# Optimization experiments

Measured on AMD Instinct MI355X. Metric: run time of the kernel, lower is better.

## Reference

```python
import jax, jax.numpy as jnp
import numpy as np

N_VOX = 200000   # active voxels
K = 27           # 3x3x3 kernel offsets
P = 100000       # rulebook pairs per kernel offset
C_IN = 64
C_OUT = 64
BN_EPS = 1e-5


def setup_inputs() -> dict:
    key = jax.random.key(0)
    k1, k2, k3, k4, k5 = jax.random.split(key, 5)
    features = jax.random.normal(k1, (N_VOX, C_IN), dtype=jnp.float32)
    weight = jax.random.normal(k2, (K, C_IN, C_OUT), dtype=jnp.float32) * 0.05
    bias = jax.random.normal(k3, (C_OUT,), dtype=jnp.float32) * 0.05
    gamma = jnp.ones((C_OUT,), dtype=jnp.float32)
    beta = jnp.zeros((C_OUT,), dtype=jnp.float32)
    in_idx = jax.random.randint(k4, (K, P), 0, N_VOX, dtype=jnp.int32)
    out_idx = jax.random.randint(k5, (K, P), 0, N_VOX, dtype=jnp.int32)
    return {"features": features, "weight": weight, "bias": bias,
            "gamma": gamma, "beta": beta, "in_idx": in_idx, "out_idx": out_idx}


def reference(features, weight, bias, gamma, beta, in_idx, out_idx):
    # --- sparse submanifold conv: gather -> per-offset GEMM -> scatter-add ---
    gathered = features[in_idx]                         # [K, P, C_in]
    partial = jnp.einsum('kpc,kcd->kpd', gathered, weight)  # [K, P, C_out]
    out = jnp.zeros((N_VOX, C_OUT), dtype=features.dtype)
    out = out.at[out_idx.reshape(-1)].add(partial.reshape(-1, C_OUT))
    out = out + bias                                    # conv bias
    # --- BatchNorm1d (training mode: batch stats, biased variance) ---
    mean = jnp.mean(out, axis=0)
    var = jnp.mean(jnp.square(out - mean), axis=0)
    normed = (out - mean) * jax.lax.rsqrt(var + BN_EPS) * gamma + beta
    # --- ReLU ---
    return jnp.maximum(normed, 0.0)
```

## Files before the change

### kernel.cpp

```cpp
#include <hip/hip_runtime.h>
#include <hip/hip_bf16.h>

#define N_VOX 200000
#define KOFF 27
#define PPK 100000
#define C 64
#define BN_EPS 1e-5f

typedef __bf16 bf16x8 __attribute__((ext_vector_type(8)));
typedef __bf16 bf16x4 __attribute__((ext_vector_type(4)));
typedef float f32x4 __attribute__((ext_vector_type(4)));

__global__ __launch_bounds__(256)
void convert_features(const float* __restrict__ f, __bf16* __restrict__ fb)
{
    const size_t total4 = (size_t)N_VOX * C / 4;
    const size_t i = (size_t)blockIdx.x * blockDim.x + threadIdx.x;
    if (i >= total4) return;
    const float4 v = ((const float4*)f)[i];
    bf16x4 o;
    o.x = (__bf16)v.x; o.y = (__bf16)v.y; o.z = (__bf16)v.z; o.w = (__bf16)v.w;
    ((bf16x4*)fb)[i] = o;
}

__global__ __launch_bounds__(256)
void convert_weight(const float* __restrict__ w, __bf16* __restrict__ wt)
{
    const int k = blockIdx.x;
    const float* W = w + (size_t)k * C * C;
    __bf16* Wt = wt + (size_t)k * C * C;
    for (int idx = threadIdx.x; idx < C * C; idx += 256) {
        const int ci = idx >> 6, co = idx & 63;
        Wt[co * C + ci] = (__bf16)W[idx];
    }
}

__global__ __launch_bounds__(256)
void hist_kernel(const int* __restrict__ out_idx, unsigned* __restrict__ counts,
                 int k0, int npair)
{
    const int i = blockIdx.x * 256 + threadIdx.x;
    if (i < npair) {
        const int o = out_idx[(size_t)k0 * PPK + i];
        atomicAdd(&counts[o], 1u);
    }
}

__global__ __launch_bounds__(256)
void scan1(const unsigned* __restrict__ counts, unsigned* __restrict__ offsets,
           unsigned* __restrict__ bsums)
{
    __shared__ unsigned sdata[256];
    const int t = threadIdx.x;
    const int base = blockIdx.x * 1024 + t * 4;
    unsigned v[4]; unsigned s = 0;
#pragma unroll
    for (int u = 0; u < 4; ++u) {
        v[u] = (base + u < N_VOX) ? counts[base + u] : 0u;
        s += v[u];
    }
    sdata[t] = s;
    __syncthreads();
    for (int off = 1; off < 256; off <<= 1) {
        const unsigned add = (t >= off) ? sdata[t - off] : 0u;
        __syncthreads();
        sdata[t] += add;
        __syncthreads();
    }
    const unsigned incl = sdata[t];
    unsigned run = incl - s;
    if (t == 255) bsums[blockIdx.x] = incl;
#pragma unroll
    for (int u = 0; u < 4; ++u) {
        if (base + u < N_VOX) offsets[base + u] = run;
        run += v[u];
    }
}

__global__ __launch_bounds__(256)
void scan2(unsigned* __restrict__ bsums, int nb)
{
    __shared__ unsigned sdata[256];
    const int t = threadIdx.x;
    const unsigned s = (t < nb) ? bsums[t] : 0u;
    sdata[t] = s;
    __syncthreads();
    for (int off = 1; off < 256; off <<= 1) {
        const unsigned add = (t >= off) ? sdata[t - off] : 0u;
        __syncthreads();
        sdata[t] += add;
        __syncthreads();
    }
    if (t < nb) bsums[t] = sdata[t] - s;
}

__global__ __launch_bounds__(256)
void scan3(unsigned* __restrict__ offsets, const unsigned* __restrict__ bsums,
           unsigned* __restrict__ cursor)
{
    const int i = blockIdx.x * 256 + threadIdx.x;
    if (i < N_VOX) {
        const unsigned v = offsets[i] + bsums[i >> 10];
        offsets[i] = v;
        cursor[i] = v;
    }
}

__global__ __launch_bounds__(256)
void rank_fill(const int* __restrict__ out_idx, unsigned* __restrict__ cursor,
               unsigned* __restrict__ rank, int k0, int npair)
{
    const int i = blockIdx.x * 256 + threadIdx.x;
    if (i < npair) {
        const int o = out_idx[(size_t)k0 * PPK + i];
        rank[i] = atomicAdd(&cursor[o], 1u);
    }
}

__global__ __launch_bounds__(256)
void conv_scatter(const __bf16* __restrict__ featb, const __bf16* __restrict__ wtb,
                  const int* __restrict__ in_idx, const unsigned* __restrict__ rank,
                  __bf16* __restrict__ partial, int k0)
{
    constexpr int TP = 256;
    constexpr int STRIDE = 72;
    __shared__ __bf16 sA[TP * STRIDE];
    __shared__ unsigned s_rank[TP];

    const int kloc = blockIdx.y;
    const int k = k0 + kloc;
    const int tile_base = blockIdx.x * TP;
    const int t = threadIdx.x;
    const int lane = t & 63;
    const int wave = t >> 6;
    const int m16 = lane & 15;
    const int quad = lane >> 4;

    const __bf16* Wt = wtb + (size_t)k * C * C;
    bf16x8 bfrag[4][2];
#pragma unroll
    for (int nt = 0; nt < 4; ++nt)
#pragma unroll
        for (int kc = 0; kc < 2; ++kc)
            bfrag[nt][kc] = *(const bf16x8*)(Wt + (nt * 16 + m16) * C + kc * 32 + quad * 8);

    {
        const int pair = tile_base + t;
        s_rank[t] = (pair < PPK) ? rank[(size_t)kloc * PPK + pair] : 0u;
    }

    const int c8 = t & 7;
    const int r0 = t >> 3;
#pragma unroll
    for (int it = 0; it < 8; ++it) {
        const int r = r0 + it * 32;
        const int pair = tile_base + r;
        const int row = (pair < PPK) ? in_idx[(size_t)k * PPK + pair] : 0;
        const float4 v = *(const float4*)(featb + (size_t)row * C + c8 * 8);
        *(float4*)(sA + r * STRIDE + c8 * 8) = v;
    }
    __syncthreads();

    f32x4 acc[4][4] = {};
    const int mbase = wave * 64;
#pragma unroll
    for (int kc = 0; kc < 2; ++kc) {
        bf16x8 afrag[4];
#pragma unroll
        for (int mt = 0; mt < 4; ++mt)
            afrag[mt] = *(const bf16x8*)(sA + (mbase + mt * 16 + m16) * STRIDE + kc * 32 + quad * 8);
#pragma unroll
        for (int nt = 0; nt < 4; ++nt)
#pragma unroll
            for (int mt = 0; mt < 4; ++mt)
                acc[mt][nt] = __builtin_amdgcn_mfma_f32_16x16x32_bf16(
                    afrag[mt], bfrag[nt][kc], acc[mt][nt], 0, 0, 0);
    }

#pragma unroll
    for (int mt = 0; mt < 4; ++mt) {
#pragma unroll
        for (int reg = 0; reg < 4; ++reg) {
            const int r = mbase + mt * 16 + quad * 4 + reg;
            const int pair = tile_base + r;
            if (pair < PPK) {
                const unsigned slot = s_rank[r];
                bf16x4 pv;
                pv.x = (__bf16)acc[mt][0][reg];
                pv.y = (__bf16)acc[mt][1][reg];
                pv.z = (__bf16)acc[mt][2][reg];
                pv.w = (__bf16)acc[mt][3][reg];
                *(bf16x4*)(partial + (size_t)slot * C + (m16 << 2)) = pv;
            }
        }
    }
}

__global__ __launch_bounds__(256)
void reduce_kernel(const __bf16* __restrict__ partial,
                   const unsigned* __restrict__ offsets,
                   const unsigned* __restrict__ counts,
                   float* __restrict__ out, const int first)
{
    const int t = threadIdx.x;
    const int j = t & 15;
    const int i = t >> 4;
    const int o = blockIdx.x * 16 + i;
    const unsigned beg = offsets[o];
    const unsigned cnt = counts[o];
    float a0, a1, a2, a3;
    if (first) {
        a0 = a1 = a2 = a3 = 0.f;
    } else {
        a0 = out[(size_t)o * C + j];
        a1 = out[(size_t)o * C + 16 + j];
        a2 = out[(size_t)o * C + 32 + j];
        a3 = out[(size_t)o * C + 48 + j];
    }
    const __bf16* base = partial + (size_t)beg * C + (j << 2);
    for (unsigned e = 0; e < cnt; ++e) {
        const bf16x4 v = *(const bf16x4*)(base + (size_t)e * C);
        a0 += (float)v.x; a1 += (float)v.y; a2 += (float)v.z; a3 += (float)v.w;
    }
    out[(size_t)o * C + j]      = a0;
    out[(size_t)o * C + 16 + j] = a1;
    out[(size_t)o * C + 32 + j] = a2;
    out[(size_t)o * C + 48 + j] = a3;
}

__global__ __launch_bounds__(256)
void conv_mfma(const __bf16* __restrict__ featb, const __bf16* __restrict__ wtb,
               const int* __restrict__ in_idx, const int* __restrict__ out_idx,
               float* __restrict__ out)
{
    constexpr int TP = 256;
    constexpr int STRIDE = 72;
    __shared__ __bf16 sA[TP * STRIDE];
    __shared__ int s_out[TP];

    const int k = blockIdx.y;
    const int tile_base = blockIdx.x * TP;
    const int t = threadIdx.x;
    const int lane = t & 63;
    const int wave = t >> 6;
    const int m16 = lane & 15;
    const int quad = lane >> 4;

    const __bf16* Wt = wtb + (size_t)k * C * C;
    bf16x8 bfrag[4][2];
#pragma unroll
    for (int nt = 0; nt < 4; ++nt)
#pragma unroll
        for (int kc = 0; kc < 2; ++kc)
            bfrag[nt][kc] = *(const bf16x8*)(Wt + (nt * 16 + m16) * C + kc * 32 + quad * 8);

    {
        const int pair = tile_base + t;
        s_out[t] = (pair < PPK) ? out_idx[(size_t)k * PPK + pair] : 0;
    }

    const int c8 = t & 7;
    const int r0 = t >> 3;
#pragma unroll
    for (int it = 0; it < 8; ++it) {
        const int r = r0 + it * 32;
        const int pair = tile_base + r;
        const int row = (pair < PPK) ? in_idx[(size_t)k * PPK + pair] : 0;
        const float4 v = *(const float4*)(featb + (size_t)row * C + c8 * 8);
        *(float4*)(sA + r * STRIDE + c8 * 8) = v;
    }
    __syncthreads();

    f32x4 acc[4][4] = {};
    const int mbase = wave * 64;
#pragma unroll
    for (int kc = 0; kc < 2; ++kc) {
        bf16x8 afrag[4];
#pragma unroll
        for (int mt = 0; mt < 4; ++mt)
            afrag[mt] = *(const bf16x8*)(sA + (mbase + mt * 16 + m16) * STRIDE + kc * 32 + quad * 8);
#pragma unroll
        for (int nt = 0; nt < 4; ++nt)
#pragma unroll
            for (int mt = 0; mt < 4; ++mt)
                acc[mt][nt] = __builtin_amdgcn_mfma_f32_16x16x32_bf16(
                    afrag[mt], bfrag[nt][kc], acc[mt][nt], 0, 0, 0);
    }

#pragma unroll
    for (int mt = 0; mt < 4; ++mt) {
#pragma unroll
        for (int reg = 0; reg < 4; ++reg) {
            const int r = mbase + mt * 16 + quad * 4 + reg;
            const int pair = tile_base + r;
            if (pair < PPK) {
                const int o = s_out[r];
                float* orow = out + (size_t)o * C + m16;
#pragma unroll
                for (int nt = 0; nt < 4; ++nt)
                    unsafeAtomicAdd(orow + nt * 16, acc[mt][nt][reg]);
            }
        }
    }
}

__global__ __launch_bounds__(256)
void stats_kernel(const float* __restrict__ out,
                  float* __restrict__ stats,
                  int rows_per_block)
{
    __shared__ float ssum[256];
    __shared__ float ssq[256];
    const int c   = threadIdx.x & 63;
    const int sub = threadIdx.x >> 6;
    const int row0 = blockIdx.x * rows_per_block;
    const int row1 = min(row0 + rows_per_block, N_VOX);
    float s = 0.f, q = 0.f;
    for (int r = row0 + sub; r < row1; r += 4) {
        const float v = out[(size_t)r * C + c];
        s += v;
        q += v * v;
    }
    ssum[threadIdx.x] = s;
    ssq[threadIdx.x]  = q;
    __syncthreads();
    if (sub == 0) {
        s = ssum[c] + ssum[64 + c] + ssum[128 + c] + ssum[192 + c];
        q = ssq[c]  + ssq[64 + c]  + ssq[128 + c]  + ssq[192 + c];
        unsafeAtomicAdd(&stats[c], s);
        unsafeAtomicAdd(&stats[64 + c], q);
    }
}

__global__ void finalize_params(const float* __restrict__ stats,
                                const float* __restrict__ gamma,
                                const float* __restrict__ beta,
                                float* __restrict__ ss)
{
    const int c = threadIdx.x;
    const float inv_n = 1.0f / (float)N_VOX;
    const float mean  = stats[c] * inv_n;
    const float var   = stats[64 + c] * inv_n - mean * mean;
    const float scale = rsqrtf(var + BN_EPS) * gamma[c];
    ss[c]      = scale;
    ss[64 + c] = beta[c] - mean * scale;
}

__global__ __launch_bounds__(256)
void norm_kernel(float* __restrict__ out, const float* __restrict__ ss)
{
    const size_t total4 = (size_t)N_VOX * C / 4;
    const size_t idx = (size_t)blockIdx.x * blockDim.x + threadIdx.x;
    if (idx >= total4) return;
    const int c4 = (int)(idx & 15);
    float4 v = ((const float4*)out)[idx];
    const float4 sc = ((const float4*)ss)[c4];
    const float4 sh = ((const float4*)(ss + 64))[c4];
    v.x = fmaxf(v.x * sc.x + sh.x, 0.f);
    v.y = fmaxf(v.y * sc.y + sh.y, 0.f);
    v.z = fmaxf(v.z * sc.z + sh.z, 0.f);
    v.w = fmaxf(v.w * sc.w + sh.w, 0.f);
    ((float4*)out)[idx] = v;
}

static inline size_t align_up(size_t x) { return (x + 255) & ~(size_t)255; }

extern "C" void kernel_launch(void* const* d_in, const int* in_sizes, int n_in,
                              void* d_out, int out_size, void* d_ws, size_t ws_size,
                              hipStream_t stream)
{
    const float* features = (const float*)d_in[0];
    const float* weight   = (const float*)d_in[1];
    const float* gamma    = (const float*)d_in[3];
    const float* beta     = (const float*)d_in[4];
    const int*   in_idx   = (const int*)d_in[5];
    const int*   out_idx  = (const int*)d_in[6];
    float* out = (float*)d_out;

    char* base = (char*)d_ws;
    size_t off = 0;
    __bf16* featb = (__bf16*)(base + off); off += align_up((size_t)N_VOX * C * 2);
    __bf16* wtb   = (__bf16*)(base + off); off += align_up((size_t)KOFF * C * C * 2);
    float*  stats = (float*)(base + off);  off += align_up(128 * 4);
    float*  ss    = (float*)(base + off);  off += align_up(128 * 4);
    unsigned* counts  = (unsigned*)(base + off); off += align_up((size_t)N_VOX * 4);
    unsigned* offsets = (unsigned*)(base + off); off += align_up((size_t)N_VOX * 4);
    unsigned* cursor  = (unsigned*)(base + off); off += align_up((size_t)N_VOX * 4);
    unsigned* bsums   = (unsigned*)(base + off); off += align_up(256 * 4);
    const size_t fixed = off;

    int g_cap = 0;
    if (ws_size > fixed)
        g_cap = (int)((ws_size - fixed) / ((size_t)PPK * 132));
    if (g_cap > KOFF) g_cap = KOFF;

    hipMemsetAsync(stats, 0, 128 * sizeof(float), stream);

    const size_t total4 = (size_t)N_VOX * C / 4;
    convert_features<<<(int)((total4 + 255) / 256), 256, 0, stream>>>(features, featb);
    convert_weight<<<KOFF, 256, 0, stream>>>(weight, wtb);

    if (g_cap >= 5) {
        const int G = (KOFF + g_cap - 1) / g_cap;
        const int gmax = (KOFF + G - 1) / G;
        unsigned* rank = (unsigned*)(base + off);
        __bf16* partial = (__bf16*)(base + off + align_up((size_t)gmax * PPK * 4));
        const int gbase_sz = KOFF / G, rem = KOFF % G;
        int k0 = 0;
        for (int ci = 0; ci < G; ++ci) {
            const int g = gbase_sz + (ci < rem ? 1 : 0);
            const int np = g * PPK;
            hipMemsetAsync(counts, 0, (size_t)N_VOX * 4, stream);
            hist_kernel<<<(np + 255) / 256, 256, 0, stream>>>(out_idx, counts, k0, np);
            scan1<<<(N_VOX + 1023) / 1024, 256, 0, stream>>>(counts, offsets, bsums);
            scan2<<<1, 256, 0, stream>>>(bsums, (N_VOX + 1023) / 1024);
            scan3<<<(N_VOX + 255) / 256, 256, 0, stream>>>(offsets, bsums, cursor);
            rank_fill<<<(np + 255) / 256, 256, 0, stream>>>(out_idx, cursor, rank, k0, np);
            dim3 cgrid((PPK + 255) / 256, g);
            conv_scatter<<<cgrid, 256, 0, stream>>>(featb, wtb, in_idx, rank, partial, k0);
            reduce_kernel<<<N_VOX / 16, 256, 0, stream>>>(partial, offsets, counts, out,
                                                          ci == 0 ? 1 : 0);
            k0 += g;
        }
    } else {
        hipMemsetAsync(out, 0, (size_t)N_VOX * C * sizeof(float), stream);
        dim3 cgrid((PPK + 255) / 256, KOFF);
        conv_mfma<<<cgrid, 256, 0, stream>>>(featb, wtb, in_idx, out_idx, out);
    }

    const int rpb = (N_VOX + 511) / 512;
    stats_kernel<<<512, 256, 0, stream>>>(out, stats, rpb);

    finalize_params<<<1, 64, 0, stream>>>(stats, gamma, beta, ss);

    norm_kernel<<<(int)((total4 + 255) / 256), 256, 0, stream>>>(out, ss);
}
```

Measured before the change: 681.5 us.

## Fuse rank assignment into conv scatter, swizzle LDS, and parallelize reduce

Removes the separate rank_fill kernel and rank buffer by doing the cursor atomicAdd inside conv_scatter and broadcasting ranks via wave shuffles. Replaces padded LDS rows with an XOR swizzle, uses nontemporal stores and loads for the partial buffer, and folds the counts reset into scan1 so only one memset is needed. The reduce kernel now uses one wave per voxel with four partial rows read in parallel and a shuffle reduction, using offset differences instead of counts. This saves kernel launches and memory traffic, at the cost of more atomic pressure inside the GEMM kernel and larger workspace groups.

```diff
diff --git a/kernel.cpp b/kernel.cpp
--- a/kernel.cpp
+++ b/kernel.cpp
@@ -47,7 +47,7 @@
 }
 
 __global__ __launch_bounds__(256)
-void scan1(const unsigned* __restrict__ counts, unsigned* __restrict__ offsets,
+void scan1(unsigned* __restrict__ counts, unsigned* __restrict__ offsets,
            unsigned* __restrict__ bsums)
 {
     __shared__ unsigned sdata[256];
@@ -56,7 +56,9 @@
     unsigned v[4]; unsigned s = 0;
 #pragma unroll
     for (int u = 0; u < 4; ++u) {
-        v[u] = (base + u < N_VOX) ? counts[base + u] : 0u;
+        const bool ok = (base + u < N_VOX);
+        v[u] = ok ? counts[base + u] : 0u;
+        if (ok) counts[base + u] = 0u;
         s += v[u];
     }
     sdata[t] = s;
@@ -107,28 +109,15 @@
 }
 
 __global__ __launch_bounds__(256)
-void rank_fill(const int* __restrict__ out_idx, unsigned* __restrict__ cursor,
-               unsigned* __restrict__ rank, int k0, int npair)
-{
-    const int i = blockIdx.x * 256 + threadIdx.x;
-    if (i < npair) {
-        const int o = out_idx[(size_t)k0 * PPK + i];
-        rank[i] = atomicAdd(&cursor[o], 1u);
-    }
-}
-
-__global__ __launch_bounds__(256)
 void conv_scatter(const __bf16* __restrict__ featb, const __bf16* __restrict__ wtb,
-                  const int* __restrict__ in_idx, const unsigned* __restrict__ rank,
-                  __bf16* __restrict__ partial, int k0)
+                  const int* __restrict__ in_idx, const int* __restrict__ out_idx,
+                  unsigned* __restrict__ cursor, __bf16* __restrict__ partial,
+                  int k0)
 {
     constexpr int TP = 256;
-    constexpr int STRIDE = 72;
-    __shared__ __bf16 sA[TP * STRIDE];
-    __shared__ unsigned s_rank[TP];
-
-    const int kloc = blockIdx.y;
-    const int k = k0 + kloc;
+    __shared__ __bf16 sA[TP * 64];
+
+    const int k = k0 + blockIdx.y;
     const int tile_base = blockIdx.x * TP;
     const int t = threadIdx.x;
     const int lane = t & 63;
@@ -144,9 +133,13 @@
         for (int kc = 0; kc < 2; ++kc)
             bfrag[nt][kc] = *(const bf16x8*)(Wt + (nt * 16 + m16) * C + kc * 32 + quad * 8);
 
+    unsigned my_rank = 0u;
     {
         const int pair = tile_base + t;
-        s_rank[t] = (pair < PPK) ? rank[(size_t)kloc * PPK + pair] : 0u;
+        if (pair < PPK) {
+            const int o = out_idx[(size_t)k * PPK + pair];
+            my_rank = atomicAdd(&cursor[o], 1u);
+        }
     }
 
     const int c8 = t & 7;
@@ -157,7 +150,7 @@
         const int pair = tile_base + r;
         const int row = (pair < PPK) ? in_idx[(size_t)k * PPK + pair] : 0;
         const float4 v = *(const float4*)(featb + (size_t)row * C + c8 * 8);
-        *(float4*)(sA + r * STRIDE + c8 * 8) = v;
+        *(float4*)(sA + r * 64 + ((c8 ^ (r0 & 7)) << 3)) = v;
     }
     __syncthreads();
 
@@ -168,7 +161,8 @@
         bf16x8 afrag[4];
 #pragma unroll
         for (int mt = 0; mt < 4; ++mt)
-            afrag[mt] = *(const bf16x8*)(sA + (mbase + mt * 16 + m16) * STRIDE + kc * 32 + quad * 8);
+            afrag[mt] = *(const bf16x8*)(sA + (mbase + mt * 16 + m16) * 64
+                                         + ((((kc << 2) | quad) ^ (m16 & 7)) << 3));
 #pragma unroll
         for (int nt = 0; nt < 4; ++nt)
 #pragma unroll
@@ -181,16 +175,17 @@
     for (int mt = 0; mt < 4; ++mt) {
 #pragma unroll
         for (int reg = 0; reg < 4; ++reg) {
-            const int r = mbase + mt * 16 + quad * 4 + reg;
-            const int pair = tile_base + r;
+            const int rloc = mt * 16 + quad * 4 + reg;
+            const unsigned slot = __shfl(my_rank, rloc, 64);
+            const int pair = tile_base + mbase + rloc;
             if (pair < PPK) {
-                const unsigned slot = s_rank[r];
                 bf16x4 pv;
                 pv.x = (__bf16)acc[mt][0][reg];
                 pv.y = (__bf16)acc[mt][1][reg];
                 pv.z = (__bf16)acc[mt][2][reg];
                 pv.w = (__bf16)acc[mt][3][reg];
-                *(bf16x4*)(partial + (size_t)slot * C + (m16 << 2)) = pv;
+                __builtin_nontemporal_store(
+                    pv, (bf16x4*)(partial + (size_t)slot * C + (m16 << 2)));
             }
         }
     }
@@ -199,33 +194,37 @@
 __global__ __launch_bounds__(256)
 void reduce_kernel(const __bf16* __restrict__ partial,
                    const unsigned* __restrict__ offsets,
-                   const unsigned* __restrict__ counts,
-                   float* __restrict__ out, const int first)
-{
-    const int t = threadIdx.x;
-    const int j = t & 15;
-    const int i = t >> 4;
-    const int o = blockIdx.x * 16 + i;
+                   float* __restrict__ out, const int first, const unsigned np)
+{
+    const int wave = threadIdx.x >> 6;
+    const int lane = threadIdx.x & 63;
+    const int e = lane >> 4;
+    const int j = lane & 15;
+    const int o = blockIdx.x * 4 + wave;
+    if (o >= N_VOX) return;
     const unsigned beg = offsets[o];
-    const unsigned cnt = counts[o];
-    float a0, a1, a2, a3;
-    if (first) {
-        a0 = a1 = a2 = a3 = 0.f;
-    } else {
-        a0 = out[(size_t)o * C + j];
-        a1 = out[(size_t)o * C + 16 + j];
-        a2 = out[(size_t)o * C + 32 + j];
-        a3 = out[(size_t)o * C + 48 + j];
-    }
-    const __bf16* base = partial + (size_t)beg * C + (j << 2);
-    for (unsigned e = 0; e < cnt; ++e) {
-        const bf16x4 v = *(const bf16x4*)(base + (size_t)e * C);
+    const unsigned end = (o + 1 < N_VOX) ? offsets[o + 1] : np;
+    float a0 = 0.f, a1 = 0.f, a2 = 0.f, a3 = 0.f;
+    for (unsigned s = beg + e; s < end; s += 4) {
+        const bf16x4 v = __builtin_nontemporal_load(
+            (const bf16x4*)(partial + (size_t)s * C + (j << 2)));
         a0 += (float)v.x; a1 += (float)v.y; a2 += (float)v.z; a3 += (float)v.w;
     }
-    out[(size_t)o * C + j]      = a0;
-    out[(size_t)o * C + 16 + j] = a1;
-    out[(size_t)o * C + 32 + j] = a2;
-    out[(size_t)o * C + 48 + j] = a3;
+#pragma unroll
+    for (int mask = 16; mask <= 32; mask <<= 1) {
+        a0 += __shfl_xor(a0, mask, 64);
+        a1 += __shfl_xor(a1, mask, 64);
+        a2 += __shfl_xor(a2, mask, 64);
+        a3 += __shfl_xor(a3, mask, 64);
+    }
+    if (e == 0) {
+        float* orow = out + (size_t)o * C;
+        if (first) {
+            orow[j] = a0; orow[16 + j] = a1; orow[32 + j] = a2; orow[48 + j] = a3;
+        } else {
+            orow[j] += a0; orow[16 + j] += a1; orow[32 + j] += a2; orow[48 + j] += a3;
+        }
+    }
 }
 
 __global__ __launch_bounds__(256)
@@ -391,7 +390,7 @@
 
     int g_cap = 0;
     if (ws_size > fixed)
-        g_cap = (int)((ws_size - fixed) / ((size_t)PPK * 132));
+        g_cap = (int)((ws_size - fixed) / ((size_t)PPK * 128));
     if (g_cap > KOFF) g_cap = KOFF;
 
     hipMemsetAsync(stats, 0, 128 * sizeof(float), stream);
@@ -402,24 +401,23 @@
 
     if (g_cap >= 5) {
         const int G = (KOFF + g_cap - 1) / g_cap;
-        const int gmax = (KOFF + G - 1) / G;
-        unsigned* rank = (unsigned*)(base + off);
-        __bf16* partial = (__bf16*)(base + off + align_up((size_t)gmax * PPK * 4));
+        __bf16* partial = (__bf16*)(base + off);
         const int gbase_sz = KOFF / G, rem = KOFF % G;
+        hipMemsetAsync(counts, 0, (size_t)N_VOX * 4, stream);
         int k0 = 0;
         for (int ci = 0; ci < G; ++ci) {
             const int g = gbase_sz + (ci < rem ? 1 : 0);
             const int np = g * PPK;
-            hipMemsetAsync(counts, 0, (size_t)N_VOX * 4, stream);
             hist_kernel<<<(np + 255) / 256, 256, 0, stream>>>(out_idx, counts, k0, np);
             scan1<<<(N_VOX + 1023) / 1024, 256, 0, stream>>>(counts, offsets, bsums);
             scan2<<<1, 256, 0, stream>>>(bsums, (N_VOX + 1023) / 1024);
             scan3<<<(N_VOX + 255) / 256, 256, 0, stream>>>(offsets, bsums, cursor);
-            rank_fill<<<(np + 255) / 256, 256, 0, stream>>>(out_idx, cursor, rank, k0, np);
             dim3 cgrid((PPK + 255) / 256, g);
-            conv_scatter<<<cgrid, 256, 0, stream>>>(featb, wtb, in_idx, rank, partial, k0);
-            reduce_kernel<<<N_VOX / 16, 256, 0, stream>>>(partial, offsets, counts, out,
-                                                          ci == 0 ? 1 : 0);
+            conv_scatter<<<cgrid, 256, 0, stream>>>(featb, wtb, in_idx, out_idx,
+                                                    cursor, partial, k0);
+            reduce_kernel<<<(N_VOX + 3) / 4, 256, 0, stream>>>(partial, offsets, out,
+                                                               ci == 0 ? 1 : 0,
+                                                               (unsigned)np);
             k0 += g;
         }
     } else {
```

New measurement: 680.5 us. No clear change (-0.2%).
